# Kernel tuning notes

Measured on AMD Instinct MI355X. Metric: run time of the kernel, lower is better.

Reference implementation:

```python
import jax, jax.numpy as jnp
import numpy as np
import math

DIM = 2048; H = 16; QR = 1536; KVR = 512; DN = 128; DR = 64; DV = 128
BS = 4; S = 1024
QK_HEAD = DN + DR  # 192


def _rms(x, w, eps=1e-6):
    v = jnp.mean(x * x, axis=-1, keepdims=True)
    return w * (x * jax.lax.rsqrt(v + eps))


def _rope_cos_sin(seq_len, dim):
    inv_freq = 1.0 / (10000.0 ** (jnp.arange(0, dim, 2, dtype=jnp.float32) / dim))
    t = jnp.arange(seq_len, dtype=jnp.float32)
    freqs = jnp.einsum('s,d->sd', t, inv_freq)
    freqs = jnp.concatenate([freqs, freqs], axis=-1)  # [S, dim]
    return jnp.cos(freqs), jnp.sin(freqs)


def _rotate_half(x):
    x1, x2 = jnp.split(x, 2, axis=-1)
    return jnp.concatenate([-x2, x1], axis=-1)


def setup_inputs() -> dict:
    key = jax.random.key(0)
    ks = jax.random.split(key, 12)
    sd = 0.02
    x = jax.random.normal(ks[0], (BS, S, DIM), dtype=jnp.float32)
    # causal additive mask [b, s, t]
    i = jnp.arange(S)
    causal = jnp.where(i[:, None] >= i[None, :], 0.0, -1e9).astype(jnp.float32)
    mask = jnp.broadcast_to(causal, (BS, S, S))
    return {
        'x': x,
        'mask': mask,
        'wq_a_w': jax.random.normal(ks[1], (QR, DIM)) * sd,
        'wq_a_b': jnp.zeros((QR,), jnp.float32),
        'q_norm_w': jnp.ones((QR,), jnp.float32),
        'wq_b_w': jax.random.normal(ks[2], (H * QK_HEAD, QR)) * sd,
        'wq_b_b': jnp.zeros((H * QK_HEAD,), jnp.float32),
        'wkv_a_w': jax.random.normal(ks[3], (KVR + DR, DIM)) * sd,
        'wkv_a_b': jnp.zeros((KVR + DR,), jnp.float32),
        'kv_norm_w': jnp.ones((KVR,), jnp.float32),
        'wkv_b_w': jax.random.normal(ks[4], (H * (DN + DV), KVR)) * sd,
        'wo_w': jax.random.normal(ks[5], (DIM, H * DV)) * sd,
        'wo_b': jnp.zeros((DIM,), jnp.float32),
    }


def reference(x, mask, wq_a_w, wq_a_b, q_norm_w, wq_b_w, wq_b_b,
              wkv_a_w, wkv_a_b, kv_norm_w, wkv_b_w, wo_w, wo_b):
    bs, seq_len, _ = x.shape
    # Q low-rank path
    q = x @ wq_a_w.T + wq_a_b                     # [b,s,QR]
    q = _rms(q, q_norm_w)
    q = q @ wq_b_w.T + wq_b_b                     # [b,s,H*192]
    q = q.reshape(bs, seq_len, H, QK_HEAD)
    q_nope, q_pe = q[..., :DN], q[..., DN:]       # [b,s,h,128], [b,s,h,64]
    # compressed KV path
    kv = x @ wkv_a_w.T + wkv_a_b                  # [b,s,KVR+64]
    c, k_pe = kv[..., :KVR], kv[..., KVR:]        # [b,s,512], [b,s,64]
    # RoPE on the rope sub-dims
    cos, sin = _rope_cos_sin(seq_len, DR)         # [s,64]
    cos4 = cos[None, :, None, :]
    sin4 = sin[None, :, None, :]
    q_pe = q_pe * cos4 + _rotate_half(q_pe) * sin4
    k_pe4 = k_pe[:, :, None, :]
    k_pe = (k_pe4 * cos4 + _rotate_half(k_pe4) * sin4)[:, :, 0, :]  # [b,s,64]
    # weight absorption: wkv_b viewed [H, DN+DV, KVR]
    wkv_b = wkv_b_w.reshape(H, DN + DV, KVR)
    q_abs = jnp.einsum('bshd,hdc->bshc', q_nope, wkv_b[:, :DN])      # [b,s,h,512]
    c_n = _rms(c, kv_norm_w)                                         # [b,t,512]
    scores = (jnp.einsum('bshc,btc->bsht', q_abs, c_n)
              + jnp.einsum('bshr,btr->bsht', q_pe, k_pe)) / math.sqrt(QK_HEAD)
    scores = scores + mask[:, :, None, :]
    scores = jax.nn.softmax(scores, axis=-1)
    o = jnp.einsum('bsht,btc->bshc', scores, c_n)                    # [b,s,h,512]
    o = jnp.einsum('bshc,hdc->bshd', o, wkv_b[:, -DV:])              # [b,s,h,128]
    o = o.reshape(bs, seq_len, H * DV)
    return o @ wo_w.T + wo_b
```

## Files before the change

kernel.cpp:

```cpp
#include <hip/hip_runtime.h>


typedef __attribute__((ext_vector_type(8))) short bf16x8;
typedef __attribute__((ext_vector_type(4))) float f32x4;
typedef __attribute__((ext_vector_type(4))) int i32x4;
typedef unsigned short ushort_t;
typedef unsigned int uint32;

typedef const __attribute__((address_space(1))) void* gas_ptr;
typedef __attribute__((address_space(3))) void* las_ptr;

#define DEV __device__ __forceinline__
#define WAITVM(N) asm volatile("s_waitcnt vmcnt(" #N ")" ::: "memory")

DEV float b2f(ushort_t u) { return __uint_as_float(((uint32)u) << 16); }
DEV ushort_t f2b(float f) {
  uint32 u = __float_as_uint(f);
  return (ushort_t)((u + 0x7fffu + ((u >> 16) & 1u)) >> 16);
}
DEV uint32 pkb(float lo, float hi) { return (uint32)f2b(lo) | ((uint32)f2b(hi) << 16); }

__global__ __launch_bounds__(256) void cast_k(const float4* __restrict__ in,
                                              ushort4* __restrict__ out, int n4) {
  int i = blockIdx.x * 256 + threadIdx.x;
  if (i < n4) {
    float4 v = in[i];
    ushort4 o; o.x = f2b(v.x); o.y = f2b(v.y); o.z = f2b(v.z); o.w = f2b(v.w);
    out[i] = o;
  }
}

__global__ __launch_bounds__(256) void cast_vb_k(const float* __restrict__ in,
                                                 ushort_t* __restrict__ out, int dofs) {
  int i4 = blockIdx.x * 256 + threadIdx.x;
  int c4 = i4 & 127, d = (i4 >> 7) & 127, h = i4 >> 14;
  const float4 v = *(const float4*)(in + ((long)(h * 256 + dofs + d)) * 512 + c4 * 4);
  ushort4 o; o.x = f2b(v.x); o.y = f2b(v.y); o.z = f2b(v.z); o.w = f2b(v.w);
  ((ushort4*)out)[i4] = o;
}

DEV float block_reduce_sum(float v, float* sbuf) {
#pragma unroll
  for (int d = 32; d >= 1; d >>= 1) v += __shfl_xor(v, d);
  if ((threadIdx.x & 63) == 0) sbuf[threadIdx.x >> 6] = v;
  __syncthreads();
  return sbuf[0] + sbuf[1] + sbuf[2] + sbuf[3];
}

__global__ __launch_bounds__(256) void rms_1536_k(const float* __restrict__ in,
                                                  ushort_t* __restrict__ out,
                                                  const float* __restrict__ w) {
  __shared__ float sbuf[4];
  long row = blockIdx.x;
  const float* p = in + row * 1536;
  float v[6]; float ss = 0.f;
#pragma unroll
  for (int i = 0; i < 6; ++i) { v[i] = p[threadIdx.x + i * 256]; ss += v[i] * v[i]; }
  ss = block_reduce_sum(ss, sbuf);
  float sc = rsqrtf(ss * (1.0f / 1536.0f) + 1e-6f);
#pragma unroll
  for (int i = 0; i < 6; ++i) {
    int c = threadIdx.x + i * 256;
    out[row * 1536 + c] = f2b(v[i] * sc * w[c]);
  }
}

__global__ __launch_bounds__(256) void kv_post_k(const float* __restrict__ in,
                                                 ushort_t* __restrict__ out,
                                                 const float* __restrict__ w) {
  __shared__ float sbuf[4];
  long row = blockIdx.x; int tid = threadIdx.x;
  const float* p = in + row * 576;
  float v0 = p[tid], v1 = p[tid + 256];
  float ss = block_reduce_sum(v0 * v0 + v1 * v1, sbuf);
  float sc = rsqrtf(ss * (1.0f / 512.0f) + 1e-6f);
  out[row * 576 + tid] = f2b(v0 * sc * w[tid]);
  out[row * 576 + tid + 256] = f2b(v1 * sc * w[tid + 256]);
  if (tid < 32) {
    int t = (int)(row & 1023);
    float x1 = p[512 + tid], x2 = p[544 + tid];
    float ang = (float)t * powf(10000.0f, -(float)tid * (1.0f / 32.0f));
    float s, c; sincosf(ang, &s, &c);
    out[row * 576 + 512 + tid] = f2b(x1 * c - x2 * s);
    out[row * 576 + 544 + tid] = f2b(x2 * c + x1 * s);
  }
}

__global__ __launch_bounds__(256) void krope_k(const ushort_t* __restrict__ kcat,
                                               ushort_t* __restrict__ kabs) {
  long row = blockIdx.x; int tid = threadIdx.x;
  int j = tid & 63;
  ushort_t v = kcat[row * 576 + 512 + j];
  for (int h = tid >> 6; h < 16; h += 4)
    kabs[((long)h * 4096 + row) * 192 + 128 + j] = v;
}

__global__ __launch_bounds__(512) void vtp_k(const ushort_t* __restrict__ kcat,
                                             ushort_t* __restrict__ vtp) {
  int vc = threadIdx.x;
  int tb = blockIdx.x;
  int b = blockIdx.y;
  const ushort_t* src = kcat + ((long)(b * 1024 + tb * 8)) * 576 + vc;
  ushort_t tmp[8];
#pragma unroll
  for (int jj = 0; jj < 8; ++jj) tmp[jj] = src[jj * 576];
  *(uint4*)(vtp + (((long)b * 128 + tb) * 512 + vc) * 8) = *(uint4*)tmp;
}

__global__ __launch_bounds__(256) void split_rope_q_k(const float* __restrict__ q,
                                                      ushort_t* __restrict__ qcat2) {
  const float RS = 0.07216878364870322f;
  long row = blockIdx.x; int tid = threadIdx.x;
  const float* p = q + row * 3072;
#pragma unroll
  for (int i = 0; i < 8; ++i) {
    int idx = tid + i * 256;
    int h = idx >> 7, d = idx & 127;
    qcat2[((long)h * 4096 + row) * 192 + d] = f2b(p[h * 192 + d] * RS);
  }
  int t = (int)(row & 1023);
#pragma unroll
  for (int i = 0; i < 2; ++i) {
    int idx = tid + i * 256;
    int h = idx >> 5, j = idx & 31;
    float x1 = p[h * 192 + 128 + j], x2 = p[h * 192 + 160 + j];
    float ang = (float)t * powf(10000.0f, -(float)j * (1.0f / 32.0f));
    float s, c; sincosf(ang, &s, &c);
    long base = ((long)h * 4096 + row) * 192;
    qcat2[base + 128 + j] = f2b((x1 * c - x2 * s) * RS);
    qcat2[base + 160 + j] = f2b((x2 * c + x1 * s) * RS);
  }
}

template <bool OUT_BF16>
__global__ __launch_bounds__(256) void gemm_bt_k(
    const ushort_t* __restrict__ A, int lda, long sAz,
    const ushort_t* __restrict__ B, int ldb, long sBz,
    void* __restrict__ C, int ldc, long sCz,
    const float* __restrict__ bias, float scale,
    int M, int N, int K) {
  __shared__ ushort_t As[2 * 4096];
  __shared__ ushort_t Bs[2 * 4096];
  int tid = threadIdx.x;
  int wave = tid >> 6, lane = tid & 63;
  int row0 = blockIdx.x * 128, col0 = blockIdx.y * 128;
  int z = blockIdx.z;
  const ushort_t* Az = A + (long)z * sAz;
  const ushort_t* Bz = B + (long)z * sBz;
  int wr = wave >> 1, wc = wave & 1;
  int lr = lane & 15, kq = lane >> 4;

  f32x4 acc[4][4];
#pragma unroll
  for (int m = 0; m < 4; ++m)
#pragma unroll
    for (int n = 0; n < 4; ++n) acc[m][n] = (f32x4){0.f, 0.f, 0.f, 0.f};

  auto stage = [&](int buf, int k0) {
#pragma unroll
    for (int rnd = 0; rnd < 2; ++rnd) {
      int e = rnd * 2048 + wave * 512 + lane * 8;
      int tr = e >> 5, tc = e & 31;
      int ar = row0 + tr; if (ar >= M) ar = M - 1;
      int br = col0 + tr; if (br >= N) br = N - 1;
      __builtin_amdgcn_global_load_lds((gas_ptr)(Az + (long)ar * lda + (k0 + tc)),
          (las_ptr)(As + buf * 4096 + rnd * 2048 + wave * 512), 16, 0, 0);
      __builtin_amdgcn_global_load_lds((gas_ptr)(Bz + (long)br * ldb + (k0 + tc)),
          (las_ptr)(Bs + buf * 4096 + rnd * 2048 + wave * 512), 16, 0, 0);
    }
  };

  stage(0, 0);
  int nk = K >> 5;
  for (int kt = 0; kt < nk; ++kt) {
    int cur = kt & 1;
    if (kt + 1 < nk) { stage(cur ^ 1, (kt + 1) * 32); WAITVM(4); }
    else { WAITVM(0); }
    __builtin_amdgcn_s_barrier();
    __builtin_amdgcn_sched_barrier(0);
    const ushort_t* Ac = As + cur * 4096;
    const ushort_t* Bc = Bs + cur * 4096;
    bf16x8 a[4], bb[4];
#pragma unroll
    for (int m = 0; m < 4; ++m)
      a[m] = *(const bf16x8*)(Ac + (wr * 64 + m * 16 + lr) * 32 + kq * 8);
#pragma unroll
    for (int n = 0; n < 4; ++n)
      bb[n] = *(const bf16x8*)(Bc + (wc * 64 + n * 16 + lr) * 32 + kq * 8);
#pragma unroll
    for (int m = 0; m < 4; ++m)
#pragma unroll
      for (int n = 0; n < 4; ++n)
        acc[m][n] = __builtin_amdgcn_mfma_f32_16x16x32_bf16(a[m], bb[n], acc[m][n], 0, 0, 0);
    __builtin_amdgcn_s_barrier();
  }

#pragma unroll
  for (int n = 0; n < 4; ++n) {
    int gcol = col0 + wc * 64 + n * 16 + lr;
    if (gcol >= N) continue;
    float bv = bias ? bias[gcol] : 0.f;
#pragma unroll
    for (int m = 0; m < 4; ++m) {
      int gr0 = row0 + wr * 64 + m * 16 + kq * 4;
#pragma unroll
      for (int r = 0; r < 4; ++r) {
        int gr = gr0 + r;
        if (gr < M) {
          float v = acc[m][n][r] * scale + bv;
          long ci = (long)z * sCz + (long)gr * ldc + gcol;
          if constexpr (OUT_BF16) ((ushort_t*)C)[ci] = f2b(v);
          else ((float*)C)[ci] = v;
        }
      }
    }
  }
}

__global__ __launch_bounds__(512, 1) void flash5_k(const ushort_t* __restrict__ qcat2,
                                                   const ushort_t* __restrict__ kabs,
                                                   const ushort_t* __restrict__ vtp,
                                                   ushort_t* __restrict__ O) {
  __shared__ __align__(16) ushort_t SMEM[2 * 6400 + 2 * 16384];

  int tid = threadIdx.x;
  int wave = tid >> 6, lane = tid & 63;
  int lr = lane & 15, kq = lane >> 4;
  int bi = blockIdx.x;
  int jz = bi >> 6;
  int qb = (jz < 4) ? jz : 11 - jz;
  int bh = bi & 63;
  int h = bh >> 2, b = bh & 3;
  int s0 = qb * 128;
  int nt = (qb + 1) * 4;

  const ushort_t* kt = kabs + ((long)h * 4096 + b * 1024) * 192;
  const ushort_t* vt = vtp + (long)b * 524288;
  const ushort_t* qp = qcat2 + ((long)(h * 4096 + b * 1024 + s0 + wave * 16 + lr)) * 192 + kq * 8;

  auto stageK = [&](int buf, int t0) {
    const ushort_t* sb = kt + (long)t0 * 192;
    ushort_t* kb = SMEM + buf * 6400;
#pragma unroll
    for (int ii = 0; ii < 2; ++ii) {
      int c = ii * 512 + tid;
      if (ii == 1 && tid >= 288) break;
      int t = (int)((unsigned)c / 25u);
      int r = c - t * 25;
      int rr = (r == 24) ? 0 : r;
      const ushort_t* src = sb + t * 192 + rr * 8;
      __builtin_amdgcn_global_load_lds((gas_ptr)src, (las_ptr)(kb + c * 8), 16, 0, 0);
    }
  };
  auto stageV = [&](int buf, int t0) {
    const ushort_t* sb = vt + (long)(t0 >> 3) * 4096;
    ushort_t* vb = SMEM + 12800 + buf * 16384;
#pragma unroll
    for (int ii = 0; ii < 4; ++ii) {
      int c0 = (ii * 8 + wave) * 64;
      const ushort_t* src = sb + (long)(c0 + lane) * 8;
      __builtin_amdgcn_global_load_lds((gas_ptr)src, (las_ptr)(vb + c0 * 8), 16, 0, 0);
    }
  };

  stageK(0, 0); stageV(0, 0);
  bf16x8 qreg[6];
#pragma unroll
  for (int st = 0; st < 6; ++st) qreg[st] = *(const bf16x8*)(qp + st * 32);

  f32x4 o[32];
#pragma unroll
  for (int v = 0; v < 32; ++v) o[v] = (f32x4){0.f, 0.f, 0.f, 0.f};
  float m_run = -1e30f, l_run = 0.f;

  int row_g = s0 + wave * 16 + lr;
  int idx_lo = (((kq & 1) << 5) + lr) << 2;
  int idx_hi = idx_lo + 64;
  bool losel = (kq < 2);

  __syncthreads();

  for (int it = 0; it < nt; ++it) {
    int cur = it & 1;
    if (it + 1 < nt) { stageK(cur ^ 1, (it + 1) * 32); stageV(cur ^ 1, (it + 1) * 32); }
    const ushort_t* Kc = SMEM + cur * 6400;
    f32x4 sv0 = (f32x4){0.f, 0.f, 0.f, 0.f}, sv1 = sv0;
    __builtin_amdgcn_s_setprio(1);
#pragma unroll
    for (int st = 0; st < 6; ++st) {
      int off = st * 32 + kq * 8;
      bf16x8 k0 = *(const bf16x8*)(Kc + lr * 200 + off);
      bf16x8 k1 = *(const bf16x8*)(Kc + (16 + lr) * 200 + off);
      sv0 = __builtin_amdgcn_mfma_f32_16x16x32_bf16(k0, qreg[st], sv0, 0, 0, 0);
      sv1 = __builtin_amdgcn_mfma_f32_16x16x32_bf16(k1, qreg[st], sv1, 0, 0, 0);
    }
    __builtin_amdgcn_s_setprio(0);
    int t0 = it * 32;
    if (t0 >= s0) {
#pragma unroll
      for (int rr = 0; rr < 4; ++rr) {
        if (t0 + kq * 4 + rr > row_g) sv0[rr] = -1e30f;
        if (t0 + 16 + kq * 4 + rr > row_g) sv1[rr] = -1e30f;
      }
    }
    float mx = fmaxf(fmaxf(fmaxf(sv0[0], sv0[1]), fmaxf(sv0[2], sv0[3])),
                     fmaxf(fmaxf(sv1[0], sv1[1]), fmaxf(sv1[2], sv1[3])));
    mx = fmaxf(mx, __shfl_xor(mx, 16));
    mx = fmaxf(mx, __shfl_xor(mx, 32));
    float mn = fmaxf(m_run, mx);
    float alpha = __expf(m_run - mn);
    float p0 = __expf(sv0[0] - mn), p1 = __expf(sv0[1] - mn);
    float p2 = __expf(sv0[2] - mn), p3 = __expf(sv0[3] - mn);
    float p4 = __expf(sv1[0] - mn), p5 = __expf(sv1[1] - mn);
    float p6 = __expf(sv1[2] - mn), p7 = __expf(sv1[3] - mn);
    float psum = ((p0 + p1) + (p2 + p3)) + ((p4 + p5) + (p6 + p7));
    psum += __shfl_xor(psum, 16);
    psum += __shfl_xor(psum, 32);
    l_run = l_run * alpha + psum;
    m_run = mn;
    int u0 = (int)pkb(p0, p1), u1 = (int)pkb(p2, p3);
    int u2 = (int)pkb(p4, p5), u3 = (int)pkb(p6, p7);
    int b00 = __builtin_amdgcn_ds_bpermute(idx_lo, u0);
    int b10 = __builtin_amdgcn_ds_bpermute(idx_lo, u1);
    int b20 = __builtin_amdgcn_ds_bpermute(idx_lo, u2);
    int b30 = __builtin_amdgcn_ds_bpermute(idx_lo, u3);
    int b01 = __builtin_amdgcn_ds_bpermute(idx_hi, u0);
    int b11 = __builtin_amdgcn_ds_bpermute(idx_hi, u1);
    int b21 = __builtin_amdgcn_ds_bpermute(idx_hi, u2);
    int b31 = __builtin_amdgcn_ds_bpermute(idx_hi, u3);
    i32x4 w;
    w.x = losel ? b00 : b20; w.y = losel ? b10 : b30;
    w.z = losel ? b01 : b21; w.w = losel ? b11 : b31;
    bf16x8 pa = __builtin_bit_cast(bf16x8, w);
    float a0 = __shfl(alpha, kq * 4 + 0), a1 = __shfl(alpha, kq * 4 + 1);
    float a2 = __shfl(alpha, kq * 4 + 2), a3 = __shfl(alpha, kq * 4 + 3);
    if (__any((a0 != 1.f) | (a1 != 1.f) | (a2 != 1.f) | (a3 != 1.f))) {
      f32x4 av; av[0] = a0; av[1] = a1; av[2] = a2; av[3] = a3;
#pragma unroll
      for (int v = 0; v < 32; ++v) o[v] *= av;
    }
    const ushort_t* Vc = SMEM + 12800 + cur * 16384 + (kq * 512 + lr) * 8;
    __builtin_amdgcn_s_setprio(1);
#pragma unroll
    for (int v = 0; v < 32; ++v) {
      bf16x8 bv = *(const bf16x8*)(Vc + v * 128);
      o[v] = __builtin_amdgcn_mfma_f32_16x16x32_bf16(pa, bv, o[v], 0, 0, 0);
    }
    __builtin_amdgcn_s_setprio(0);
    __syncthreads();
  }
  float l0 = __shfl(l_run, kq * 4 + 0), l1 = __shfl(l_run, kq * 4 + 1);
  float l2 = __shfl(l_run, kq * 4 + 2), l3 = __shfl(l_run, kq * 4 + 3);
  f32x4 inv; inv[0] = 1.f / l0; inv[1] = 1.f / l1; inv[2] = 1.f / l2; inv[3] = 1.f / l3;
  ushort_t* ob = O + ((long)(h * 4096 + b * 1024 + s0 + wave * 16 + kq * 4)) * 512 + lr;
#pragma unroll
  for (int rr = 0; rr < 4; ++rr) {
    ushort_t* orow = ob + (long)rr * 512;
#pragma unroll
    for (int v = 0; v < 32; ++v) orow[v * 16] = f2b(o[v][rr] * inv[rr]);
  }
}

extern "C" void kernel_launch(void* const* d_in, const int* in_sizes, int n_in,
                              void* d_out, int out_size, void* d_ws, size_t ws_size,
                              hipStream_t stream) {
  (void)in_sizes; (void)n_in;
  const float* x         = (const float*)d_in[0];
  const float* wq_a_w    = (const float*)d_in[2];
  const float* wq_a_b    = (const float*)d_in[3];
  const float* q_norm_w  = (const float*)d_in[4];
  const float* wq_b_w    = (const float*)d_in[5];
  const float* wq_b_b    = (const float*)d_in[6];
  const float* wkv_a_w   = (const float*)d_in[7];
  const float* wkv_a_b   = (const float*)d_in[8];
  const float* kv_norm_w = (const float*)d_in[9];
  const float* wkv_b_w   = (const float*)d_in[10];
  const float* wo_w      = (const float*)d_in[11];
  const float* wo_b      = (const float*)d_in[12];

  char* ws = (char*)d_ws;
  constexpr size_t OFF_XB     = 0;
  constexpr size_t OFF_WQA    = 16777216;
  constexpr size_t OFF_WQB    = 23068672;
  constexpr size_t OFF_QA     = 32505856;
  constexpr size_t OFF_QAN    = 57671680;
  constexpr size_t OFF_QF     = 70254592;
  constexpr size_t OFF_O      = 32505856;
  constexpr size_t OFF_O2     = 99614720;
  constexpr size_t OFF_QCAT2  = 120586240;
  constexpr size_t OFF_WKVA   = 145752064;
  constexpr size_t OFF_WKVBN  = 148111360;
  constexpr size_t OFF_WKVBV  = 150208512;
  constexpr size_t OFF_WO     = 152305664;
  constexpr size_t OFF_KVF    = 160694272;
  constexpr size_t OFF_KCAT   = 170131456;
  constexpr size_t OFF_VTP    = 174850048;
  constexpr size_t OFF_KABS   = 179044352;
  constexpr size_t WS_NEED    = 204210176;
  if (ws_size < WS_NEED) {
    (void)hipMemsetAsync(d_out, 0, (size_t)out_size * sizeof(float), stream);
    return;
  }

  ushort_t* xb     = (ushort_t*)(ws + OFF_XB);
  ushort_t* wqa    = (ushort_t*)(ws + OFF_WQA);
  ushort_t* wqb    = (ushort_t*)(ws + OFF_WQB);
  float*    qa     = (float*)(ws + OFF_QA);
  ushort_t* qan    = (ushort_t*)(ws + OFF_QAN);
  float*    qf     = (float*)(ws + OFF_QF);
  ushort_t* Obuf   = (ushort_t*)(ws + OFF_O);
  ushort_t* o2     = (ushort_t*)(ws + OFF_O2);
  ushort_t* qcat2  = (ushort_t*)(ws + OFF_QCAT2);
  ushort_t* wkva   = (ushort_t*)(ws + OFF_WKVA);
  ushort_t* wkvbn  = (ushort_t*)(ws + OFF_WKVBN);
  ushort_t* wkvbv  = (ushort_t*)(ws + OFF_WKVBV);
  ushort_t* wo     = (ushort_t*)(ws + OFF_WO);
  float*    kvf    = (float*)(ws + OFF_KVF);
  ushort_t* kcat   = (ushort_t*)(ws + OFF_KCAT);
  ushort_t* vtp    = (ushort_t*)(ws + OFF_VTP);
  ushort_t* kabs   = (ushort_t*)(ws + OFF_KABS);

  cast_k<<<8192, 256, 0, stream>>>((const float4*)x, (ushort4*)xb, 2097152);
  cast_k<<<3072, 256, 0, stream>>>((const float4*)wq_a_w, (ushort4*)wqa, 786432);
  cast_k<<<4608, 256, 0, stream>>>((const float4*)wq_b_w, (ushort4*)wqb, 1179648);
  cast_k<<<1152, 256, 0, stream>>>((const float4*)wkv_a_w, (ushort4*)wkva, 294912);
  cast_k<<<4096, 256, 0, stream>>>((const float4*)wo_w, (ushort4*)wo, 1048576);
  cast_vb_k<<<1024, 256, 0, stream>>>(wkv_b_w, wkvbv, 128);
  cast_vb_k<<<1024, 256, 0, stream>>>(wkv_b_w, wkvbn, 0);

  gemm_bt_k<false><<<dim3(32, 12, 1), 256, 0, stream>>>(xb, 2048, 0, wqa, 2048, 0,
      qa, 1536, 0, wq_a_b, 1.f, 4096, 1536, 2048);
  rms_1536_k<<<4096, 256, 0, stream>>>(qa, qan, q_norm_w);
  gemm_bt_k<false><<<dim3(32, 24, 1), 256, 0, stream>>>(qan, 1536, 0, wqb, 1536, 0,
      qf, 3072, 0, wq_b_b, 1.f, 4096, 3072, 1536);
  gemm_bt_k<false><<<dim3(32, 5, 1), 256, 0, stream>>>(xb, 2048, 0, wkva, 2048, 0,
      kvf, 576, 0, wkv_a_b, 1.f, 4096, 576, 2048);
  split_rope_q_k<<<4096, 256, 0, stream>>>(qf, qcat2);
  kv_post_k<<<4096, 256, 0, stream>>>(kvf, kcat, kv_norm_w);
  vtp_k<<<dim3(128, 4), 512, 0, stream>>>(kcat, vtp);
  krope_k<<<4096, 256, 0, stream>>>(kcat, kabs);
  gemm_bt_k<true><<<dim3(32, 1, 16), 256, 0, stream>>>(kcat, 576, 0,
      wkvbn, 512, (long)128 * 512, kabs, 192, (long)4096 * 192,
      nullptr, 1.f, 4096, 128, 512);
  flash5_k<<<512, 512, 0, stream>>>(qcat2, kabs, vtp, Obuf);
  gemm_bt_k<true><<<dim3(32, 1, 16), 256, 0, stream>>>(Obuf, 512, (long)4096 * 512,
      wkvbv, 512, (long)128 * 512, o2, 2048, 128, nullptr, 1.f, 4096, 128, 512);
  gemm_bt_k<false><<<dim3(32, 16, 1), 256, 0, stream>>>(o2, 2048, 0, wo, 2048, 0,
      (float*)d_out, 2048, 0, wo_b, 1.f, 4096, 2048, 2048);
}
```

Before: 419.7 us.

## Fuse KV post-processing kernels, fold Q RoPE into GEMM epilogue, add BK=64 GEMM

Merges kv_post, krope and vtp transpose into one kernel that processes eight rows per block, using wave shuffles and an LDS transpose. Adds a new GEMM with a 64-wide K tile, swizzled LDS and 16x16x32 MFMA. Its epilogue writes the Q projection directly into the head-major, scaled, RoPE-rotated qcat2 layout, which removes the fp32 qf round trip and the split_rope kernel. The intent is to cut kernel launches and intermediate memory traffic, at the cost of more LDS per GEMM block and sincos work in the epilogue.

```diff
diff --git a/kernel.cpp b/kernel.cpp
--- a/kernel.cpp
+++ b/kernel.cpp
@@ -65,71 +65,52 @@
   }
 }
 
-__global__ __launch_bounds__(256) void kv_post_k(const float* __restrict__ in,
-                                                 ushort_t* __restrict__ out,
-                                                 const float* __restrict__ w) {
-  __shared__ float sbuf[4];
-  long row = blockIdx.x; int tid = threadIdx.x;
-  const float* p = in + row * 576;
-  float v0 = p[tid], v1 = p[tid + 256];
-  float ss = block_reduce_sum(v0 * v0 + v1 * v1, sbuf);
+__global__ __launch_bounds__(512) void kvfuse_k(const float* __restrict__ kvf,
+                                                const float* __restrict__ w,
+                                                ushort_t* __restrict__ kcat,
+                                                ushort_t* __restrict__ vtp,
+                                                ushort_t* __restrict__ kabs) {
+  __shared__ ushort_t sh[8 * 512];
+  int tid = threadIdx.x, wv = tid >> 6, lane = tid & 63;
+  long row = (long)blockIdx.x * 8 + wv;
+  const float* p = kvf + row * 576;
+  float4 v0 = *(const float4*)(p + lane * 8);
+  float4 v1 = *(const float4*)(p + lane * 8 + 4);
+  float ss = v0.x * v0.x + v0.y * v0.y + v0.z * v0.z + v0.w * v0.w
+           + v1.x * v1.x + v1.y * v1.y + v1.z * v1.z + v1.w * v1.w;
+#pragma unroll
+  for (int d = 1; d <= 32; d <<= 1) ss += __shfl_xor(ss, d);
   float sc = rsqrtf(ss * (1.0f / 512.0f) + 1e-6f);
-  out[row * 576 + tid] = f2b(v0 * sc * w[tid]);
-  out[row * 576 + tid + 256] = f2b(v1 * sc * w[tid + 256]);
-  if (tid < 32) {
+  float4 w0 = *(const float4*)(w + lane * 8);
+  float4 w1 = *(const float4*)(w + lane * 8 + 4);
+  ushort_t tmp[8];
+  tmp[0] = f2b(v0.x * sc * w0.x); tmp[1] = f2b(v0.y * sc * w0.y);
+  tmp[2] = f2b(v0.z * sc * w0.z); tmp[3] = f2b(v0.w * sc * w0.w);
+  tmp[4] = f2b(v1.x * sc * w1.x); tmp[5] = f2b(v1.y * sc * w1.y);
+  tmp[6] = f2b(v1.z * sc * w1.z); tmp[7] = f2b(v1.w * sc * w1.w);
+  *(uint4*)(kcat + row * 576 + lane * 8) = *(uint4*)tmp;
+  *(uint4*)(sh + wv * 512 + lane * 8) = *(uint4*)tmp;
+  if (lane < 32) {
     int t = (int)(row & 1023);
-    float x1 = p[512 + tid], x2 = p[544 + tid];
-    float ang = (float)t * powf(10000.0f, -(float)tid * (1.0f / 32.0f));
+    float x1 = p[512 + lane], x2 = p[544 + lane];
+    float ang = (float)t * powf(10000.0f, -(float)lane * (1.0f / 32.0f));
     float s, c; sincosf(ang, &s, &c);
-    out[row * 576 + 512 + tid] = f2b(x1 * c - x2 * s);
-    out[row * 576 + 544 + tid] = f2b(x2 * c + x1 * s);
-  }
-}
-
-__global__ __launch_bounds__(256) void krope_k(const ushort_t* __restrict__ kcat,
-                                               ushort_t* __restrict__ kabs) {
-  long row = blockIdx.x; int tid = threadIdx.x;
-  int j = tid & 63;
-  ushort_t v = kcat[row * 576 + 512 + j];
-  for (int h = tid >> 6; h < 16; h += 4)
-    kabs[((long)h * 4096 + row) * 192 + 128 + j] = v;
-}
-
-__global__ __launch_bounds__(512) void vtp_k(const ushort_t* __restrict__ kcat,
-                                             ushort_t* __restrict__ vtp) {
-  int vc = threadIdx.x;
-  int tb = blockIdx.x;
-  int b = blockIdx.y;
-  const ushort_t* src = kcat + ((long)(b * 1024 + tb * 8)) * 576 + vc;
-  ushort_t tmp[8];
-#pragma unroll
-  for (int jj = 0; jj < 8; ++jj) tmp[jj] = src[jj * 576];
-  *(uint4*)(vtp + (((long)b * 128 + tb) * 512 + vc) * 8) = *(uint4*)tmp;
-}
-
-__global__ __launch_bounds__(256) void split_rope_q_k(const float* __restrict__ q,
-                                                      ushort_t* __restrict__ qcat2) {
-  const float RS = 0.07216878364870322f;
-  long row = blockIdx.x; int tid = threadIdx.x;
-  const float* p = q + row * 3072;
-#pragma unroll
-  for (int i = 0; i < 8; ++i) {
-    int idx = tid + i * 256;
-    int h = idx >> 7, d = idx & 127;
-    qcat2[((long)h * 4096 + row) * 192 + d] = f2b(p[h * 192 + d] * RS);
-  }
-  int t = (int)(row & 1023);
-#pragma unroll
-  for (int i = 0; i < 2; ++i) {
-    int idx = tid + i * 256;
-    int h = idx >> 5, j = idx & 31;
-    float x1 = p[h * 192 + 128 + j], x2 = p[h * 192 + 160 + j];
-    float ang = (float)t * powf(10000.0f, -(float)j * (1.0f / 32.0f));
-    float s, c; sincosf(ang, &s, &c);
-    long base = ((long)h * 4096 + row) * 192;
-    qcat2[base + 128 + j] = f2b((x1 * c - x2 * s) * RS);
-    qcat2[base + 160 + j] = f2b((x2 * c + x1 * s) * RS);
-  }
+    ushort_t r1 = f2b(x1 * c - x2 * s), r2 = f2b(x2 * c + x1 * s);
+    kcat[row * 576 + 512 + lane] = r1;
+    kcat[row * 576 + 544 + lane] = r2;
+#pragma unroll
+    for (int h = 0; h < 16; ++h) {
+      long base = ((long)h * 4096 + row) * 192;
+      kabs[base + 128 + lane] = r1;
+      kabs[base + 160 + lane] = r2;
+    }
+  }
+  __syncthreads();
+  ushort_t t8[8];
+#pragma unroll
+  for (int j = 0; j < 8; ++j) t8[j] = sh[j * 512 + tid];
+  int b = blockIdx.x >> 7, tb = blockIdx.x & 127;
+  *(uint4*)(vtp + (((long)b * 128 + tb) * 512 + tid) * 8) = *(uint4*)t8;
 }
 
 template <bool OUT_BF16>
@@ -211,6 +192,133 @@
           long ci = (long)z * sCz + (long)gr * ldc + gcol;
           if constexpr (OUT_BF16) ((ushort_t*)C)[ci] = f2b(v);
           else ((float*)C)[ci] = v;
+        }
+      }
+    }
+  }
+}
+
+template <int MODE>
+__global__ __launch_bounds__(256) void gemm64_k(
+    const ushort_t* __restrict__ A, int lda,
+    const ushort_t* __restrict__ B, int ldb,
+    void* __restrict__ C, int ldc,
+    const float* __restrict__ bias,
+    int M, int N, int K) {
+  __shared__ ushort_t As[2 * 8192];
+  __shared__ ushort_t Bs[2 * 8192];
+  int tid = threadIdx.x;
+  int wave = tid >> 6, lane = tid & 63;
+  int row0 = blockIdx.x * 128, col0 = blockIdx.y * 128;
+  int wr = wave >> 1, wc = wave & 1;
+  int lr = lane & 15, kq = lane >> 4;
+  int rsw = lr & 7;
+
+  f32x4 acc[4][4];
+#pragma unroll
+  for (int m = 0; m < 4; ++m)
+#pragma unroll
+    for (int n = 0; n < 4; ++n) acc[m][n] = (f32x4){0.f, 0.f, 0.f, 0.f};
+
+  auto stage = [&](int buf, int k0) {
+#pragma unroll
+    for (int ii = 0; ii < 4; ++ii) {
+      int e = ii * 256 + tid;
+      int r = e >> 3, c = e & 7;
+      int scol = ((c ^ (r & 7)) << 3);
+      int ar = row0 + r; if (ar >= M) ar = M - 1;
+      int br = col0 + r; if (br >= N) br = N - 1;
+      __builtin_amdgcn_global_load_lds((gas_ptr)(A + (long)ar * lda + k0 + scol),
+          (las_ptr)(As + buf * 8192 + e * 8), 16, 0, 0);
+      __builtin_amdgcn_global_load_lds((gas_ptr)(B + (long)br * ldb + k0 + scol),
+          (las_ptr)(Bs + buf * 8192 + e * 8), 16, 0, 0);
+    }
+  };
+
+  stage(0, 0);
+  int nk = K >> 6;
+  for (int kt = 0; kt < nk; ++kt) {
+    int cur = kt & 1;
+    if (kt + 1 < nk) { stage(cur ^ 1, (kt + 1) * 64); WAITVM(8); }
+    else { WAITVM(0); }
+    __builtin_amdgcn_s_barrier();
+    __builtin_amdgcn_sched_barrier(0);
+    const ushort_t* Ac = As + cur * 8192;
+    const ushort_t* Bc = Bs + cur * 8192;
+#pragma unroll
+    for (int ks = 0; ks < 2; ++ks) {
+      bf16x8 a[4], bb[4];
+#pragma unroll
+      for (int m = 0; m < 4; ++m) {
+        int row = wr * 64 + m * 16 + lr;
+        a[m] = *(const bf16x8*)(Ac + row * 64 + ((((ks << 2) | kq) ^ rsw) << 3));
+      }
+#pragma unroll
+      for (int n = 0; n < 4; ++n) {
+        int row = wc * 64 + n * 16 + lr;
+        bb[n] = *(const bf16x8*)(Bc + row * 64 + ((((ks << 2) | kq) ^ rsw) << 3));
+      }
+#pragma unroll
+      for (int m = 0; m < 4; ++m)
+#pragma unroll
+        for (int n = 0; n < 4; ++n)
+          acc[m][n] = __builtin_amdgcn_mfma_f32_16x16x32_bf16(a[m], bb[n], acc[m][n], 0, 0, 0);
+    }
+    __builtin_amdgcn_s_barrier();
+  }
+
+  if constexpr (MODE == 0) {
+#pragma unroll
+    for (int n = 0; n < 4; ++n) {
+      int gcol = col0 + wc * 64 + n * 16 + lr;
+      if (gcol >= N) continue;
+      float bv = bias[gcol];
+#pragma unroll
+      for (int m = 0; m < 4; ++m) {
+        int gr0 = row0 + wr * 64 + m * 16 + kq * 4;
+#pragma unroll
+        for (int r = 0; r < 4; ++r) {
+          int gr = gr0 + r;
+          if (gr < M) ((float*)C)[(long)gr * ldc + gcol] = acc[m][n][r] + bv;
+        }
+      }
+    }
+  } else {
+    const float RS = 0.07216878364870322f;
+    ushort_t* qc = (ushort_t*)C;
+#pragma unroll
+    for (int n = 0; n < 4; ++n) {
+      int j = col0 + wc * 64 + n * 16 + lr;
+      int h = j / 192, d = j - h * 192;
+      if (d < 128) {
+        float bv = bias[j];
+#pragma unroll
+        for (int m = 0; m < 4; ++m) {
+          int gr0 = row0 + wr * 64 + m * 16 + kq * 4;
+#pragma unroll
+          for (int r = 0; r < 4; ++r) {
+            int gr = gr0 + r;
+            qc[((long)h * 4096 + gr) * 192 + d] = f2b((acc[m][n][r] + bv) * RS);
+          }
+        }
+      } else if (d < 160) {
+        int jj = d - 128;
+        float bv1 = bias[j], bv2 = bias[j + 32];
+        float invf = powf(10000.0f, -(float)jj * (1.0f / 32.0f));
+#pragma unroll
+        for (int m = 0; m < 4; ++m) {
+          int gr0 = row0 + wr * 64 + m * 16 + kq * 4;
+#pragma unroll
+          for (int r = 0; r < 4; ++r) {
+            int gr = gr0 + r;
+            int t = gr & 1023;
+            float s, c; sincosf((float)t * invf, &s, &c);
+            float x1 = acc[m][n][r] + bv1;
+            float x2 = acc[m][n + 2][r] + bv2;
+            long base = ((long)h * 4096 + gr) * 192;
+            qc[base + d] = f2b((x1 * c - x2 * s) * RS);
+            qc[base + d + 32] = f2b((x2 * c + x1 * s) * RS);
+          }
         }
       }
     }
@@ -384,7 +492,6 @@
   constexpr size_t OFF_WQB    = 23068672;
   constexpr size_t OFF_QA     = 32505856;
   constexpr size_t OFF_QAN    = 57671680;
-  constexpr size_t OFF_QF     = 70254592;
   constexpr size_t OFF_O      = 32505856;
   constexpr size_t OFF_O2     = 99614720;
   constexpr size_t OFF_QCAT2  = 120586240;
@@ -407,7 +514,6 @@
   ushort_t* wqb    = (ushort_t*)(ws + OFF_WQB);
   float*    qa     = (float*)(ws + OFF_QA);
   ushort_t* qan    = (ushort_t*)(ws + OFF_QAN);
-  float*    qf     = (float*)(ws + OFF_QF);
   ushort_t* Obuf   = (ushort_t*)(ws + OFF_O);
   ushort_t* o2     = (ushort_t*)(ws + OFF_O2);
   ushort_t* qcat2  = (ushort_t*)(ws + OFF_QCAT2);
@@ -428,23 +534,20 @@
   cast_vb_k<<<1024, 256, 0, stream>>>(wkv_b_w, wkvbv, 128);
   cast_vb_k<<<1024, 256, 0, stream>>>(wkv_b_w, wkvbn, 0);
 
-  gemm_bt_k<false><<<dim3(32, 12, 1), 256, 0, stream>>>(xb, 2048, 0, wqa, 2048, 0,
-      qa, 1536, 0, wq_a_b, 1.f, 4096, 1536, 2048);
+  gemm64_k<0><<<dim3(32, 12), 256, 0, stream>>>(xb, 2048, wqa, 2048,
+      qa, 1536, wq_a_b, 4096, 1536, 2048);
   rms_1536_k<<<4096, 256, 0, stream>>>(qa, qan, q_norm_w);
-  gemm_bt_k<false><<<dim3(32, 24, 1), 256, 0, stream>>>(qan, 1536, 0, wqb, 1536, 0,
-      qf, 3072, 0, wq_b_b, 1.f, 4096, 3072, 1536);
+  gemm64_k<2><<<dim3(32, 24), 256, 0, stream>>>(qan, 1536, wqb, 1536,
+      qcat2, 0, wq_b_b, 4096, 3072, 1536);
   gemm_bt_k<false><<<dim3(32, 5, 1), 256, 0, stream>>>(xb, 2048, 0, wkva, 2048, 0,
       kvf, 576, 0, wkv_a_b, 1.f, 4096, 576, 2048);
-  split_rope_q_k<<<4096, 256, 0, stream>>>(qf, qcat2);
-  kv_post_k<<<4096, 256, 0, stream>>>(kvf, kcat, kv_norm_w);
-  vtp_k<<<dim3(128, 4), 512, 0, stream>>>(kcat, vtp);
-  krope_k<<<4096, 256, 0, stream>>>(kcat, kabs);
+  kvfuse_k<<<512, 512, 0, stream>>>(kvf, kv_norm_w, kcat, vtp, kabs);
   gemm_bt_k<true><<<dim3(32, 1, 16), 256, 0, stream>>>(kcat, 576, 0,
       wkvbn, 512, (long)128 * 512, kabs, 192, (long)4096 * 192,
       nullptr, 1.f, 4096, 128, 512);
   flash5_k<<<512, 512, 0, stream>>>(qcat2, kabs, vtp, Obuf);
   gemm_bt_k<true><<<dim3(32, 1, 16), 256, 0, stream>>>(Obuf, 512, (long)4096 * 512,
       wkvbv, 512, (long)128 * 512, o2, 2048, 128, nullptr, 1.f, 4096, 128, 512);
-  gemm_bt_k<false><<<dim3(32, 16, 1), 256, 0, stream>>>(o2, 2048, 0, wo, 2048, 0,
-      (float*)d_out, 2048, 0, wo_b, 1.f, 4096, 2048, 2048);
-}
+  gemm64_k<0><<<dim3(32, 16), 256, 0, stream>>>(o2, 2048, wo, 2048,
+      (float*)d_out, 2048, wo_b, 4096, 2048, 2048);
+}
```

After: 415.2 us. About the same (-1.1%).
